# Optimization experiments

Hardware: AMD Instinct MI355X
Metric: run time of the kernel (lower is better)

## Reference

```python
import jax, jax.numpy as jnp
import numpy as np

VOXEL_SIZE = np.array([0.32, 0.32, 6.0], dtype=np.float32)
SPATIAL_SIZE = np.array([-74.88, 74.88, -74.88, 74.88, -3.0, 3.0], dtype=np.float32)
# voxel_spatial_size = ceil((max-min)/voxel_size) per dim -> [468, 468, 1]
GRID = np.array([int(np.ceil((SPATIAL_SIZE[2*i+1]-SPATIAL_SIZE[2*i])/VOXEL_SIZE[i])) for i in range(3)], dtype=np.int32)
# voxel origin = floor(min / voxel_size) -> [-234, -234, -1]
ORIGIN = np.floor(SPATIAL_SIZE[0::2] / VOXEL_SIZE).astype(np.int32)
VOL = int(np.prod(GRID))  # 468*468*1
# row-major id multipliers: prods[1:]+[1] -> [468, 1, 1]
SHIFT = np.array([int(np.prod(GRID[1:])), int(np.prod(GRID[2:])), 1], dtype=np.int32)
VOXEL_FEATURE_MIN = -1000.0

B, N, D_IN, MLP = 4, 100000, 16, 128


def setup_inputs() -> dict:
    key = jax.random.key(0)
    k1, k2, k3, k4, k5 = jax.random.split(key, 5)
    xy = jax.random.uniform(k1, (B, N, 2), minval=-80.0, maxval=80.0)
    z = jax.random.uniform(k2, (B, N, 1), minval=-4.0, maxval=4.0)
    point_xyz = jnp.concatenate([xy, z], axis=-1)
    point_feature = jax.random.normal(k3, (B, N, D_IN), dtype=jnp.float32)
    point_mask = jax.random.uniform(k4, (B, N)) < 0.95
    W = jax.random.normal(k5, (D_IN + 3, MLP), dtype=jnp.float32) * 0.1
    b = jnp.zeros((MLP,), dtype=jnp.float32)
    return {"point_xyz": point_xyz, "point_feature": point_feature,
            "point_mask": point_mask, "W": W, "b": b}


def reference(point_xyz, point_feature, point_mask, W, b):
    vs = jnp.asarray(VOXEL_SIZE, dtype=point_xyz.dtype)
    # PointToVoxel
    pvx_f = jnp.floor(point_xyz / vs)                      # [B,N,3] float voxel coords
    point_voxel_feature = point_xyz - pvx_f * vs           # delta within voxel
    pvx = pvx_f.astype(jnp.int32) - jnp.asarray(ORIGIN)    # shifted int voxel coords
    grid = jnp.asarray(GRID)
    in_bounds = jnp.all((pvx >= 0) & (pvx < grid), axis=-1)
    voxel_mask = in_bounds & point_mask                    # [B,N]
    vid = jnp.sum(pvx * jnp.asarray(SHIFT), axis=-1)       # [B,N]
    vid = vid + jnp.arange(B, dtype=jnp.int32)[:, None] * VOL
    vid = vid * voxel_mask.astype(jnp.int32)               # invalid -> 0
    # point net (Dense + ReLU) on [point_feature, voxel delta]
    feat = jnp.concatenate([point_feature, point_voxel_feature], axis=-1)
    mf = voxel_mask.astype(feat.dtype)[..., None]
    feat = feat * mf
    feat = jax.nn.relu(jnp.einsum('bnd,dk->bnk', feat, W) + b)
    feat = feat * mf
    # scatter-max into dense voxel grid
    seg = jax.ops.segment_max(feat.reshape(-1, MLP), vid.reshape(-1),
                              num_segments=B * VOL)
    seg = jnp.where(seg > VOXEL_FEATURE_MIN, seg, 0.0)
    # z dim is 1 -> squeezed: [B, 468, 468, MLP]
    return seg.reshape(B, int(GRID[0]), int(GRID[1]), MLP)
```

## Files before the change

### kernel.cpp

```cpp
#include <hip/hip_runtime.h>
#include <hip/hip_bf16.h>
#include <stdint.h>

#define BB   4
#define NN   100000
#define TOTAL (BB * NN)
#define DIN  16
#define DF   19
#define KO   128
#define GX   468
#define GY   468
#define VOL  (GX * GY)
#define NV   (BB * VOL)
#define CAP  16

#define WS_COUNTS   0
#define WS_PLIST    (NV)
#define WS_FLAG     (NV + NV * CAP)

__global__ __launch_bounds__(256) void prep(
    float4* __restrict__ out4,
    int4*   __restrict__ counts4,
    const uint4* __restrict__ mask_words,
    int* __restrict__ flag)
{
    if (blockIdx.x == 0) {
        __shared__ int sA, sB;
        if (threadIdx.x == 0) { sA = 0; sB = 0; }
        __syncthreads();
        int a = 0, b = 0;
        #pragma unroll
        for (int it = 0; it < 4; ++it) {
            uint4 w = mask_words[it * 256 + threadIdx.x];
            unsigned lo = (w.x & 0xFFu) | (w.y & 0xFFu) | (w.z & 0xFFu) | (w.w & 0xFFu);
            unsigned hi = (w.x & 0xFFFFFF00u) | (w.y & 0xFFFFFF00u) |
                          (w.z & 0xFFFFFF00u) | (w.w & 0xFFFFFF00u);
            if (hi) a = 1;
            if (lo) b = 1;
        }
        if (a) atomicOr(&sA, 1);
        if (b) atomicOr(&sB, 1);
        __syncthreads();
        if (threadIdx.x == 0) flag[0] = (sA && sB) ? 1 : 4;
    }

    const int stride = gridDim.x * 256;
    const int gid = blockIdx.x * 256 + threadIdx.x;
    const float4 zf = make_float4(0.f, 0.f, 0.f, 0.f);
    for (int i = gid; i < NV * (KO / 4); i += stride) out4[i] = zf;
    const int4 zi = make_int4(0, 0, 0, 0);
    for (int i = gid; i < NV / 4; i += stride) counts4[i] = zi;
}

__global__ __launch_bounds__(256) void pass1_bin(
    const float* __restrict__ xyz,
    const unsigned char* __restrict__ mask_raw,
    const int* __restrict__ flag,
    int* __restrict__ counts,
    int* __restrict__ plist)
{
    const int p = blockIdx.x * 256 + threadIdx.x;
    if (p >= TOTAL) return;
    const float x = xyz[p * 3 + 0];
    const float y = xyz[p * 3 + 1];
    const float z = xyz[p * 3 + 2];
    bool m;
    if (flag[0] == 4) m = (((const int*)mask_raw)[p] != 0);
    else              m = (mask_raw[p] != 0);
    const int ix = (int)floorf(x / 0.32f) + 234;
    const int iy = (int)floorf(y / 0.32f) + 234;
    const int iz = (int)floorf(z / 6.0f) + 1;
    const bool inb = ((unsigned)ix < (unsigned)GX) &
                     ((unsigned)iy < (unsigned)GY) &
                     (iz == 0) & m;
    if (inb) {
        const int vid = (p / NN) * VOL + ix * GY + iy;
        const int rank = atomicAdd(&counts[vid], 1);
        if (rank < CAP) plist[vid * CAP + rank] = p;
    }
}

__global__ __launch_bounds__(256) void gather_write(
    const float* __restrict__ xyz,
    const float* __restrict__ pfeat,
    const float* __restrict__ W,
    const float* __restrict__ bias,
    const int* __restrict__ counts,
    const int* __restrict__ plist,
    float* __restrict__ out)
{
    const int lane = threadIdx.x & 63;
    const int wave = (blockIdx.x * 256 + threadIdx.x) >> 6;
    const int v0 = wave * 8;

    const float2* W2 = (const float2*)W;
    float2 w[DF];
    #pragma unroll
    for (int d = 0; d < DF; ++d) w[d] = W2[d * 64 + lane];
    const float2 bb = ((const float2*)bias)[lane];

    for (int j = 0; j < 8; ++j) {
        const int v = v0 + j;
        int c = counts[v];
        if (c == 0) continue;
        c = min(c, CAP);
        const int o = v * CAP;

        float m0 = -3.0e38f, m1 = -3.0e38f;
        for (int t = 0; t < c; ++t) {
            const int p = plist[o + t];
            const float x = xyz[p * 3 + 0];
            const float y = xyz[p * 3 + 1];
            const float z = xyz[p * 3 + 2];
            float f[DF];
            const float4* pf4 = (const float4*)(pfeat + (size_t)p * DIN);
            float4 v0f = pf4[0], v1f = pf4[1], v2f = pf4[2], v3f = pf4[3];
            f[0]=v0f.x; f[1]=v0f.y; f[2]=v0f.z; f[3]=v0f.w;
            f[4]=v1f.x; f[5]=v1f.y; f[6]=v1f.z; f[7]=v1f.w;
            f[8]=v2f.x; f[9]=v2f.y; f[10]=v2f.z; f[11]=v2f.w;
            f[12]=v3f.x; f[13]=v3f.y; f[14]=v3f.z; f[15]=v3f.w;
            f[16] = x - floorf(x / 0.32f) * 0.32f;
            f[17] = y - floorf(y / 0.32f) * 0.32f;
            f[18] = z - floorf(z / 6.0f) * 6.0f;

            float a0 = bb.x, a1 = bb.y;
            #pragma unroll
            for (int d = 0; d < DF; ++d) {
                a0 = fmaf(f[d], w[d].x, a0);
                a1 = fmaf(f[d], w[d].y, a1);
            }
            m0 = fmaxf(m0, a0);
            m1 = fmaxf(m1, a1);
        }
        float2* dst = (float2*)(out + (size_t)v * KO) + lane;
        *dst = make_float2(fmaxf(m0, 0.f), fmaxf(m1, 0.f));
    }
}

extern "C" void kernel_launch(void* const* d_in, const int* in_sizes, int n_in,
                              void* d_out, int out_size, void* d_ws, size_t ws_size,
                              hipStream_t stream) {
    const float* xyz   = (const float*)d_in[0];
    const float* pfeat = (const float*)d_in[1];
    const unsigned char* mask = (const unsigned char*)d_in[2];
    const float* W     = (const float*)d_in[3];
    const float* bias  = (const float*)d_in[4];
    float* out = (float*)d_out;
    int* ws = (int*)d_ws;

    int* counts = ws + WS_COUNTS;
    int* plist  = ws + WS_PLIST;
    int* flag   = ws + WS_FLAG;

    prep<<<4096, 256, 0, stream>>>((float4*)out, (int4*)counts,
                                   (const uint4*)mask, flag);
    pass1_bin<<<(TOTAL + 255) / 256, 256, 0, stream>>>(xyz, mask, flag,
                                                       counts, plist);
    gather_write<<<NV / 32, 256, 0, stream>>>(xyz, pfeat, W, bias,
                                              counts, plist, out);
}
```

Baseline: 644.4 us.

## Fuse output zeroing into gather kernel with ballot-based occupancy per wave

Removes the separate full-grid zero fill of the output from the prep kernel. The gather kernel now writes every voxel exactly once, zeros for empty voxels and pooled features for occupied ones. Each wave covers 64 voxels, and each lane loads one count with a single coalesced load. A ballot then yields an occupancy bitmask, which also skips the weight loads for all-empty waves. This saves one full write pass over the roughly 450MB output, though each wave now walks 64 voxels serially with per-voxel shuffles.

```diff
diff --git a/kernel.cpp b/kernel.cpp
--- a/kernel.cpp
+++ b/kernel.cpp
@@ -13,14 +13,14 @@
 #define VOL  (GX * GY)
 #define NV   (BB * VOL)
 #define CAP  16
+#define NWAVES (NV / 64)
 
 #define WS_COUNTS   0
 #define WS_PLIST    (NV)
 #define WS_FLAG     (NV + NV * CAP)
 
 __global__ __launch_bounds__(256) void prep(
-    float4* __restrict__ out4,
-    int4*   __restrict__ counts4,
+    int4* __restrict__ counts4,
     const uint4* __restrict__ mask_words,
     int* __restrict__ flag)
 {
@@ -43,13 +43,8 @@
         __syncthreads();
         if (threadIdx.x == 0) flag[0] = (sA && sB) ? 1 : 4;
     }
-
-    const int stride = gridDim.x * 256;
-    const int gid = blockIdx.x * 256 + threadIdx.x;
-    const float4 zf = make_float4(0.f, 0.f, 0.f, 0.f);
-    for (int i = gid; i < NV * (KO / 4); i += stride) out4[i] = zf;
-    const int4 zi = make_int4(0, 0, 0, 0);
-    for (int i = gid; i < NV / 4; i += stride) counts4[i] = zi;
+    const int i = blockIdx.x * 256 + threadIdx.x;
+    if (i < NV / 4) counts4[i] = make_int4(0, 0, 0, 0);
 }
 
 __global__ __launch_bounds__(256) void pass1_bin(
@@ -80,7 +75,7 @@
     }
 }
 
-__global__ __launch_bounds__(256) void gather_write(
+__global__ __launch_bounds__(256) void fused_write(
     const float* __restrict__ xyz,
     const float* __restrict__ pfeat,
     const float* __restrict__ W,
@@ -90,21 +85,30 @@
     float* __restrict__ out)
 {
     const int lane = threadIdx.x & 63;
-    const int wave = (blockIdx.x * 256 + threadIdx.x) >> 6;
-    const int v0 = wave * 8;
+    const int wid  = (blockIdx.x * 256 + threadIdx.x) >> 6;
+    if (wid >= NWAVES) return;
+    const int v0 = wid * 64;
 
-    const float2* W2 = (const float2*)W;
+    const int c_mine = counts[v0 + lane];
+    const unsigned long long occ = __ballot(c_mine > 0);
+
     float2 w[DF];
-    #pragma unroll
-    for (int d = 0; d < DF; ++d) w[d] = W2[d * 64 + lane];
-    const float2 bb = ((const float2*)bias)[lane];
+    float2 bb = make_float2(0.f, 0.f);
+    if (occ) {
+        const float2* W2 = (const float2*)W;
+        #pragma unroll
+        for (int d = 0; d < DF; ++d) w[d] = W2[d * 64 + lane];
+        bb = ((const float2*)bias)[lane];
+    }
 
-    for (int j = 0; j < 8; ++j) {
-        const int v = v0 + j;
-        int c = counts[v];
-        if (c == 0) continue;
-        c = min(c, CAP);
-        const int o = v * CAP;
+    float2* dst = (float2*)(out + (size_t)v0 * KO) + lane;
+    for (int j = 0; j < 64; ++j, dst += 64) {
+        if (!((occ >> j) & 1ull)) {
+            *dst = make_float2(0.f, 0.f);
+            continue;
+        }
+        const int c = min(__shfl(c_mine, j), CAP);
+        const int o = (v0 + j) * CAP;
 
         float m0 = -3.0e38f, m1 = -3.0e38f;
         for (int t = 0; t < c; ++t) {
@@ -114,11 +118,11 @@
             const float z = xyz[p * 3 + 2];
             float f[DF];
             const float4* pf4 = (const float4*)(pfeat + (size_t)p * DIN);
-            float4 v0f = pf4[0], v1f = pf4[1], v2f = pf4[2], v3f = pf4[3];
-            f[0]=v0f.x; f[1]=v0f.y; f[2]=v0f.z; f[3]=v0f.w;
-            f[4]=v1f.x; f[5]=v1f.y; f[6]=v1f.z; f[7]=v1f.w;
-            f[8]=v2f.x; f[9]=v2f.y; f[10]=v2f.z; f[11]=v2f.w;
-            f[12]=v3f.x; f[13]=v3f.y; f[14]=v3f.z; f[15]=v3f.w;
+            float4 a = pf4[0], b = pf4[1], cc = pf4[2], dd = pf4[3];
+            f[0]=a.x;  f[1]=a.y;  f[2]=a.z;  f[3]=a.w;
+            f[4]=b.x;  f[5]=b.y;  f[6]=b.z;  f[7]=b.w;
+            f[8]=cc.x; f[9]=cc.y; f[10]=cc.z; f[11]=cc.w;
+            f[12]=dd.x; f[13]=dd.y; f[14]=dd.z; f[15]=dd.w;
             f[16] = x - floorf(x / 0.32f) * 0.32f;
             f[17] = y - floorf(y / 0.32f) * 0.32f;
             f[18] = z - floorf(z / 6.0f) * 6.0f;
@@ -132,7 +136,6 @@
             m0 = fmaxf(m0, a0);
             m1 = fmaxf(m1, a1);
         }
-        float2* dst = (float2*)(out + (size_t)v * KO) + lane;
         *dst = make_float2(fmaxf(m0, 0.f), fmaxf(m1, 0.f));
     }
 }
@@ -152,10 +155,10 @@
     int* plist  = ws + WS_PLIST;
     int* flag   = ws + WS_FLAG;
 
-    prep<<<4096, 256, 0, stream>>>((float4*)out, (int4*)counts,
-                                   (const uint4*)mask, flag);
+    prep<<<(NV / 4 + 255) / 256, 256, 0, stream>>>((int4*)counts,
+                                                   (const uint4*)mask, flag);
     pass1_bin<<<(TOTAL + 255) / 256, 256, 0, stream>>>(xyz, mask, flag,
                                                        counts, plist);
-    gather_write<<<NV / 32, 256, 0, stream>>>(xyz, pfeat, W, bias,
-                                              counts, plist, out);
+    fused_write<<<(NWAVES + 3) / 4, 256, 0, stream>>>(xyz, pfeat, W, bias,
+                                                      counts, plist, out);
 }
```

Measured after the change: 602.6 us. 6.5% less time.
